# Kernel tuning notes

Measured on AMD Instinct MI355X. Metric: run time of the kernel, lower is better.

The kernel has to match this reference:

```python
import jax, jax.numpy as jnp
import numpy as np

B, S, T = 512, 1024, 64

def setup_inputs() -> dict:
    key = jax.random.key(0)
    k1, k2, k3 = jax.random.split(key, 3)
    emissions = jax.random.normal(k1, (B, S, T), dtype=jnp.float32)
    tags = jax.random.randint(k2, (B, S), 0, T, dtype=jnp.int32)
    mask = jnp.ones((B, S), dtype=jnp.float32)
    transitions = jax.random.normal(k3, (T, T), dtype=jnp.float32)
    return {"emissions": emissions, "tags": tags, "mask": mask, "transitions": transitions}

def _gold_score(emissions, tags, mask, transitions):
    # emit score of the gold tag at each position: (B, S)
    e = jnp.take_along_axis(emissions, tags[:, :, None], axis=2)[:, :, 0]
    # NOTE: original indexes transitions[curr, prev]
    trans = transitions[tags[:, 1:], tags[:, :-1]]  # (B, S-1)
    score = e[:, 0] * mask[:, 0]
    score = score + jnp.sum((trans + e[:, 1:]) * mask[:, 1:], axis=1)
    return score

def _partition(emissions, mask, transitions):
    # init: emissions at t=0, masked (matches original, which multiplies score by mask[:,0])
    score0 = emissions[:, 0] * mask[:, 0][:, None]  # (B, T)
    emis_rest = jnp.swapaxes(emissions[:, 1:], 0, 1)  # (S-1, B, T)
    mask_rest = jnp.swapaxes(mask[:, 1:], 0, 1)       # (S-1, B)

    def step(score, xs):
        emit, m = xs  # (B, T), (B,)
        # next[b, j] = logsumexp_i(score[b, i] + transitions[i, j])
        nxt = jax.nn.logsumexp(score[:, :, None] + transitions[None, :, :], axis=1)
        score = nxt + emit * m[:, None]
        return score, None

    score, _ = jax.lax.scan(step, score0, (emis_rest, mask_rest))
    return jax.nn.logsumexp(score, axis=1)  # (B,)

def reference(emissions, tags, mask, transitions):
    gold = _gold_score(emissions, tags, mask, transitions)
    fwd = _partition(emissions, mask, transitions)
    return jnp.mean(fwd - gold)
```

## Files before the change

kernel.cpp:

```cpp
#include <hip/hip_runtime.h>

#define BB 512
#define SS 1024
#define TT 64

__device__ __forceinline__ float wsum64(float v) {
#pragma unroll
  for (int off = 32; off > 0; off >>= 1) v += __shfl_xor(v, off, 64);
  return v;
}

#define E_LIST(M) \
  M(0) M(1) M(2) M(3) M(4) M(5) M(6) M(7) \
  M(8) M(9) M(10) M(11) M(12) M(13) M(14) M(15) \
  M(16) M(17) M(18) M(19) M(20) M(21) M(22) M(23) \
  M(24) M(25) M(26) M(27) M(28) M(29) M(30) M(31) \
  M(32) M(33) M(34) M(35) M(36) M(37) M(38) M(39) \
  M(40) M(41) M(42) M(43) M(44) M(45) M(46) M(47) \
  M(48) M(49) M(50) M(51) M(52) M(53) M(54) M(55) \
  M(56) M(57) M(58) M(59) M(60) M(61) M(62) M(63)

#define RLS(i) __builtin_amdgcn_readlane(pb_, (i))
#define RLF(v, i) __int_as_float(__builtin_amdgcn_readlane(__float_as_int(v), (i)))

#define AFMA(acc, r, Ev) \
  asm("v_fma_f32 %0, %1, %2, %0" : "+v"(acc) : "s"(r), "v"(Ev));

#define QSTEP(iA, iB, iC, iD, jA, jB, jC, jD) \
  AFMA(a0, r0, E##iA) r0 = RLS(jA);           \
  AFMA(a1, r1, E##iB) r1 = RLS(jB);           \
  AFMA(a2, r2, E##iC) r2 = RLS(jC);           \
  AFMA(a3, r3, E##iD) r3 = RLS(jD);

#define QLAST(iA, iB, iC, iD) \
  AFMA(a0, r0, E##iA)         \
  AFMA(a1, r1, E##iB)         \
  AFMA(a2, r2, E##iC)         \
  AFMA(a3, r3, E##iD)

#define FMA_ALL_PIPE                                        \
  int r0 = RLS(0), r1 = RLS(1), r2 = RLS(2), r3 = RLS(3);   \
  QSTEP(0, 1, 2, 3, 4, 5, 6, 7)                             \
  QSTEP(4, 5, 6, 7, 8, 9, 10, 11)                           \
  QSTEP(8, 9, 10, 11, 12, 13, 14, 15)                       \
  QSTEP(12, 13, 14, 15, 16, 17, 18, 19)                     \
  QSTEP(16, 17, 18, 19, 20, 21, 22, 23)                     \
  QSTEP(20, 21, 22, 23, 24, 25, 26, 27)                     \
  QSTEP(24, 25, 26, 27, 28, 29, 30, 31)                     \
  QSTEP(28, 29, 30, 31, 32, 33, 34, 35)                     \
  QSTEP(32, 33, 34, 35, 36, 37, 38, 39)                     \
  QSTEP(36, 37, 38, 39, 40, 41, 42, 43)                     \
  QSTEP(40, 41, 42, 43, 44, 45, 46, 47)                     \
  QSTEP(44, 45, 46, 47, 48, 49, 50, 51)                     \
  QSTEP(48, 49, 50, 51, 52, 53, 54, 55)                     \
  QSTEP(52, 53, 54, 55, 56, 57, 58, 59)                     \
  QSTEP(56, 57, 58, 59, 60, 61, 62, 63)                     \
  QLAST(60, 61, 62, 63)

#define CRF_STEP(ev, mkv)                                                           \
  do {                                                                              \
    float f_ = __expf((ev) * (mkv));                                                \
    float pv_ = (DIR == 1) ? p * (f_ * inv) : p;                                    \
    int pb_ = __float_as_int(pv_);                                                  \
    float a0 = 0.f, a1 = 0.f, a2 = 0.f, a3 = 0.f;                                   \
    FMA_ALL_PIPE                                                                    \
    float s_ = (a0 + a1) + (a2 + a3);                                               \
    p = (DIR == 0) ? s_ * (f_ * inv) : s_;                                          \
    float rn_ = __int_as_float(__builtin_amdgcn_readfirstlane(__float_as_int(s_))); \
    inv = __builtin_amdgcn_rcpf(rn_);                                               \
    float lg_ = __logf(rn_);                                                        \
    Lacc += lg_;                                                                    \
    lastlg = lg_;                                                                   \
  } while (0)

template <int DIR>
__device__ __forceinline__ void part_run(int b, int lane, const float* __restrict__ em,
                                         const float* __restrict__ mask,
                                         const float* __restrict__ trans,
                                         float* __restrict__ outv) {
  const float* tp = trans + (DIR == 0 ? lane : lane * TT);
#define EINIT(i) float E##i = __expf((DIR == 0) ? tp[(i)*TT] : tp[(i)]);
  E_LIST(EINIT)
#undef EINIT

  const float* emb = em + (size_t)b * SS * TT;
  const float* mkb = mask + (size_t)b * SS;

  constexpr int NST = (DIR == 0) ? (SS / 2 - 1) : (SS / 2);
  constexpr int S0 = (DIR == 0) ? 1 : (SS - 1);
  constexpr int SD = (DIR == 0) ? 1 : -1;
  constexpr int NG8 = NST / 8;
  constexpr int TAIL8 = NST & 7;

  float p = (DIR == 0) ? __expf(emb[lane] * mkb[0]) : 1.0f;
  float inv = 1.0f, Lacc = 0.0f, lastlg = 0.0f;

  float ebuf[8];
#pragma unroll
  for (int k = 0; k < 8; ++k) ebuf[k] = emb[(S0 + SD * k) * TT + lane];
  const float* ep = emb + (ptrdiff_t)(S0 + SD * 8) * TT + lane;

  float mv = mkb[S0 + SD * lane];
  float mvn = 0.f;
  for (int t8 = 0; t8 < NG8; ++t8) {
    if ((t8 & 7) == 0 && t8 != 0) mv = mvn;
    if ((t8 & 7) == 5)
      mvn = mkb[S0 + SD * (((t8 >> 3) + 1) * 64 + lane)];
    const int base = (t8 & 7) * 8;
#pragma unroll
    for (int k = 0; k < 8; ++k) {
      float e = ebuf[k];
      ebuf[k] = *ep;
      ep += SD * TT;
      float mk = RLF(mv, base + k);
      CRF_STEP(e, mk);
    }
  }
  if constexpr (TAIL8 > 0) {
#pragma unroll
    for (int k = 0; k < TAIL8; ++k) {
      float e = ebuf[k];
      float mk = RLF(mv, (NG8 & 7) * 8 + k);
      CRF_STEP(e, mk);
    }
  }

  outv[b * TT + lane] = __logf(p) + (Lacc - lastlg);
}

__global__ void __launch_bounds__(64, 1)
    fused_kernel(const float* __restrict__ em, const int* __restrict__ tags,
                 const float* __restrict__ mask, const float* __restrict__ trans,
                 float* __restrict__ alpha, float* __restrict__ beta,
                 float* __restrict__ gpart) {
  const int lane = threadIdx.x;
  const int bid = blockIdx.x;
  if (bid < 2 * BB) {
    const int b = bid >> 1;
    if ((bid & 1) == 0)
      part_run<0>(b, lane, em, mask, trans, alpha);
    else
      part_run<1>(b, lane, em, mask, trans, beta);
  } else {
    const int gid = bid - 2 * BB;
    const int b = gid >> 2, q = gid & 3;
    const int* tg = tags + b * SS;
    const float* mkb = mask + (size_t)b * SS;
    const float* emb = em + (size_t)b * SS * TT;
    float part = 0.f;
#pragma unroll
    for (int i = 0; i < 4; ++i) {
      int s = q * 256 + i * 64 + lane;
      int t1 = tg[s];
      float e = emb[s * TT + t1];
      float contrib = (s == 0) ? e : (trans[t1 * TT + tg[s - 1]] + e);
      part = fmaf(contrib, mkb[s], part);
    }
    part = wsum64(part);
    if (lane == 0) gpart[gid] = part;
  }
}

__global__ void combine_kernel(const float* __restrict__ alpha, const float* __restrict__ beta,
                               const float* __restrict__ gpart, float* __restrict__ out) {
  const int b = threadIdx.x;
  const float* av = alpha + b * TT;
  const float* bv = beta + b * TT;
  float m = -3.4e38f, s = 0.f;
#pragma unroll 8
  for (int j = 0; j < TT; ++j) {
    float v = av[j] + bv[j];
    float nm = fmaxf(m, v);
    s = s * __expf(m - nm) + __expf(v - nm);
    m = nm;
  }
  float Z = m + __logf(s);
  float g = gpart[4 * b] + gpart[4 * b + 1] + gpart[4 * b + 2] + gpart[4 * b + 3];
  float val = Z - g;
  val = wsum64(val);
  __shared__ float red[8];
  if ((threadIdx.x & 63) == 0) red[threadIdx.x >> 6] = val;
  __syncthreads();
  if (threadIdx.x == 0) {
    float t = 0.f;
#pragma unroll
    for (int w = 0; w < 8; ++w) t += red[w];
    out[0] = t * (1.0f / (float)BB);
  }
}

extern "C" void kernel_launch(void* const* d_in, const int* in_sizes, int n_in,
                              void* d_out, int out_size, void* d_ws, size_t ws_size,
                              hipStream_t stream) {
  const float* em = (const float*)d_in[0];
  const int* tags = (const int*)d_in[1];
  const float* mask = (const float*)d_in[2];
  const float* trans = (const float*)d_in[3];
  float* out = (float*)d_out;

  float* alpha = (float*)d_ws;
  float* beta = alpha + BB * TT;
  float* gpart = beta + BB * TT;

  fused_kernel<<<2 * BB + 4 * BB, TT, 0, stream>>>(em, tags, mask, trans, alpha, beta, gpart);
  combine_kernel<<<1, BB, 0, stream>>>(alpha, beta, gpart, out);
}
```

Before: 346.1 us.

## Use packed fp16 dot2 for CRF recurrence matvec instead of fp32 FMAs

Stores exp(transitions) as packed fp16 pairs and packs neighboring lanes' state values into fp16 pairs via DPP, then performs the per-step 64-wide matvec with 32 v_dot2 instructions and 32 readlanes instead of 64 FMAs and 64 readlanes. Normalization now occurs before packing, with clamping to the fp16 range. This halves the serial instruction count per timestep but reduces the precision of the transition weights and state to fp16, risking accuracy loss or underflow over 1024 steps.

```diff
diff --git a/kernel.cpp b/kernel.cpp
--- a/kernel.cpp
+++ b/kernel.cpp
@@ -3,6 +3,14 @@
 #define BB 512
 #define SS 1024
 #define TT 64
+
+typedef _Float16 h2 __attribute__((ext_vector_type(2)));
+
+#if __has_builtin(__builtin_amdgcn_fdot2)
+#define FDOT2(a, b, c) __builtin_amdgcn_fdot2((a), (b), (c), false)
+#else
+#define FDOT2(a, b, c) ((c) + (float)(a).x * (float)(b).x + (float)(a).y * (float)(b).y)
+#endif
 
 __device__ __forceinline__ float wsum64(float v) {
 #pragma unroll
@@ -10,62 +18,32 @@
   return v;
 }
 
-#define E_LIST(M) \
+#define H_LIST(M) \
   M(0) M(1) M(2) M(3) M(4) M(5) M(6) M(7) \
   M(8) M(9) M(10) M(11) M(12) M(13) M(14) M(15) \
   M(16) M(17) M(18) M(19) M(20) M(21) M(22) M(23) \
-  M(24) M(25) M(26) M(27) M(28) M(29) M(30) M(31) \
-  M(32) M(33) M(34) M(35) M(36) M(37) M(38) M(39) \
-  M(40) M(41) M(42) M(43) M(44) M(45) M(46) M(47) \
-  M(48) M(49) M(50) M(51) M(52) M(53) M(54) M(55) \
-  M(56) M(57) M(58) M(59) M(60) M(61) M(62) M(63)
+  M(24) M(25) M(26) M(27) M(28) M(29) M(30) M(31)
 
-#define RLS(i) __builtin_amdgcn_readlane(pb_, (i))
 #define RLF(v, i) __int_as_float(__builtin_amdgcn_readlane(__float_as_int(v), (i)))
 
-#define AFMA(acc, r, Ev) \
-  asm("v_fma_f32 %0, %1, %2, %0" : "+v"(acc) : "s"(r), "v"(Ev));
-
-#define QSTEP(iA, iB, iC, iD, jA, jB, jC, jD) \
-  AFMA(a0, r0, E##iA) r0 = RLS(jA);           \
-  AFMA(a1, r1, E##iB) r1 = RLS(jB);           \
-  AFMA(a2, r2, E##iC) r2 = RLS(jC);           \
-  AFMA(a3, r3, E##iD) r3 = RLS(jD);
-
-#define QLAST(iA, iB, iC, iD) \
-  AFMA(a0, r0, E##iA)         \
-  AFMA(a1, r1, E##iB)         \
-  AFMA(a2, r2, E##iC)         \
-  AFMA(a3, r3, E##iD)
-
-#define FMA_ALL_PIPE                                        \
-  int r0 = RLS(0), r1 = RLS(1), r2 = RLS(2), r3 = RLS(3);   \
-  QSTEP(0, 1, 2, 3, 4, 5, 6, 7)                             \
-  QSTEP(4, 5, 6, 7, 8, 9, 10, 11)                           \
-  QSTEP(8, 9, 10, 11, 12, 13, 14, 15)                       \
-  QSTEP(12, 13, 14, 15, 16, 17, 18, 19)                     \
-  QSTEP(16, 17, 18, 19, 20, 21, 22, 23)                     \
-  QSTEP(20, 21, 22, 23, 24, 25, 26, 27)                     \
-  QSTEP(24, 25, 26, 27, 28, 29, 30, 31)                     \
-  QSTEP(28, 29, 30, 31, 32, 33, 34, 35)                     \
-  QSTEP(32, 33, 34, 35, 36, 37, 38, 39)                     \
-  QSTEP(36, 37, 38, 39, 40, 41, 42, 43)                     \
-  QSTEP(40, 41, 42, 43, 44, 45, 46, 47)                     \
-  QSTEP(44, 45, 46, 47, 48, 49, 50, 51)                     \
-  QSTEP(48, 49, 50, 51, 52, 53, 54, 55)                     \
-  QSTEP(52, 53, 54, 55, 56, 57, 58, 59)                     \
-  QSTEP(56, 57, 58, 59, 60, 61, 62, 63)                     \
-  QLAST(60, 61, 62, 63)
+#define DOTQ(q)                                                          \
+  {                                                                      \
+    int r_ = __builtin_amdgcn_readlane(pkb_, 2 * (q));                   \
+    acc_[(q)&3] = FDOT2(__builtin_bit_cast(h2, r_), Ep##q, acc_[(q)&3]); \
+  }
 
 #define CRF_STEP(ev, mkv)                                                           \
   do {                                                                              \
     float f_ = __expf((ev) * (mkv));                                                \
-    float pv_ = (DIR == 1) ? p * (f_ * inv) : p;                                    \
-    int pb_ = __float_as_int(pv_);                                                  \
-    float a0 = 0.f, a1 = 0.f, a2 = 0.f, a3 = 0.f;                                   \
-    FMA_ALL_PIPE                                                                    \
-    float s_ = (a0 + a1) + (a2 + a3);                                               \
-    p = (DIR == 0) ? s_ * (f_ * inv) : s_;                                          \
+    float w_ = (DIR == 1) ? p * (f_ * inv) : p * inv;                               \
+    w_ = fminf(w_, 60000.0f);                                                       \
+    int nb_ = __builtin_amdgcn_update_dpp(0, __float_as_int(w_), 0xB1, 0xF, 0xF, true); \
+    h2 pk_ = __builtin_bit_cast(h2, __builtin_amdgcn_cvt_pkrtz(w_, __int_as_float(nb_))); \
+    int pkb_ = __builtin_bit_cast(int, pk_);                                        \
+    float acc_[4] = {0.f, 0.f, 0.f, 0.f};                                           \
+    H_LIST(DOTQ)                                                                    \
+    float s_ = (acc_[0] + acc_[1]) + (acc_[2] + acc_[3]);                           \
+    p = (DIR == 0) ? s_ * f_ : s_;                                                  \
     float rn_ = __int_as_float(__builtin_amdgcn_readfirstlane(__float_as_int(s_))); \
     inv = __builtin_amdgcn_rcpf(rn_);                                               \
     float lg_ = __logf(rn_);                                                        \
@@ -79,8 +57,11 @@
                                          const float* __restrict__ trans,
                                          float* __restrict__ outv) {
   const float* tp = trans + (DIR == 0 ? lane : lane * TT);
-#define EINIT(i) float E##i = __expf((DIR == 0) ? tp[(i)*TT] : tp[(i)]);
-  E_LIST(EINIT)
+#define EINIT(q)                                                                   \
+  h2 Ep##q = {                                                                     \
+      (_Float16)__expf((DIR == 0) ? tp[(2 * (q)) * TT] : tp[2 * (q)]),             \
+      (_Float16)__expf((DIR == 0) ? tp[(2 * (q) + 1) * TT] : tp[2 * (q) + 1])};
+  H_LIST(EINIT)
 #undef EINIT
 
   const float* emb = em + (size_t)b * SS * TT;
```

Measured after the change: 341.8 us. About the same (-1.3%).
